# Optimization experiments

Hardware: AMD Instinct MI355X
Metric: run time of the kernel (lower is better)

Reference implementation:

```python
import jax, jax.numpy as jnp
import numpy as np

# Gating config (matches init_kwargs)
N_GROUPS = 4        # n_expert_groups
TOPK_GROUPS = 2     # n_limited_groups
TOPK = 4            # n_activated_experts
ROUTE_SCALE = 1.0


def setup_inputs() -> dict:
    key = jax.random.key(0)
    ks = jax.random.split(key, 8)
    T, D, E, I = 2048, 1024, 16, 512
    s = 0.02  # init scale for sane numerics
    return {
        "x": jax.random.normal(ks[0], (T, D), jnp.float32),
        "gate_w": jax.random.normal(ks[1], (E, D), jnp.float32) * s,
        "w1": jax.random.normal(ks[2], (E, I, D), jnp.float32) * s,
        "w2": jax.random.normal(ks[3], (E, D, I), jnp.float32) * s,
        "w3": jax.random.normal(ks[4], (E, I, D), jnp.float32) * s,
        "ws1": jax.random.normal(ks[5], (I, D), jnp.float32) * s,
        "ws2": jax.random.normal(ks[6], (D, I), jnp.float32) * s,
        "ws3": jax.random.normal(ks[7], (I, D), jnp.float32) * s,
    }


def _gate(x, gate_w):
    # GateDeepSeekV3.forward: softmax scores, group-limited routing, top-k experts.
    T = x.shape[0]
    scores = jax.nn.softmax((x @ gate_w.T).astype(jnp.float32), axis=-1)  # [T, E]
    original_scores = scores
    E = scores.shape[-1]
    # group-limited routing: keep top `TOPK_GROUPS` groups by max score (bias is None)
    s = scores.reshape(T, N_GROUPS, E // N_GROUPS)
    group_scores = s.max(axis=-1)                                  # [T, G]
    _, gidx = jax.lax.top_k(group_scores, TOPK_GROUPS)             # [T, Gk]
    mask = jnp.zeros((T, N_GROUPS), scores.dtype).at[jnp.arange(T)[:, None], gidx].set(1.0)
    s = (s * mask[:, :, None]).reshape(T, E)
    _, indices = jax.lax.top_k(s, TOPK)                            # [T, topk]
    weights = jnp.take_along_axis(original_scores, indices, axis=1) * ROUTE_SCALE
    return weights.astype(x.dtype), indices


def reference(x, gate_w, w1, w2, w3, ws1, ws2, ws3):
    T, D = x.shape
    E = w1.shape[0]
    weights, indices = _gate(x, gate_w)
    # dense [T, E] combine weights (topk indices are unique per token)
    gate_dense = jnp.zeros((T, E), x.dtype).at[jnp.arange(T)[:, None], indices].add(weights)
    # routed experts: y_t = sum_e g[t,e] * W2_e (silu(W1_e x) * (W3_e x))
    h = jax.nn.silu(jnp.einsum('td,eid->tei', x, w1)) * jnp.einsum('td,eid->tei', x, w3)
    y = jnp.einsum('tei,te,edi->td', h, gate_dense, w2)
    # shared expert MLP over all tokens
    z = (jax.nn.silu(x @ ws1.T) * (x @ ws3.T)) @ ws2.T
    return y + z
```

## Files before the change

kernel.cpp:

```cpp
#include <hip/hip_runtime.h>
#include <hip/hip_bf16.h>
#include <math.h>

typedef float v4f __attribute__((ext_vector_type(4)));
typedef short v8s __attribute__((ext_vector_type(8)));

#define T_TOK   2048
#define DDIM    1024
#define NE      16
#define IDIM    512
#define S_ROUTED 8192
#define S_ALL   10240
#define MAXTILE 104

#define OFF_TOPKI    0u
#define OFF_TOPKW    32768u
#define OFF_PART     65536u
#define OFF_CBASE    69632u
#define OFF_SEGOFF   73728u
#define OFF_NTILES   74240u
#define OFF_TROW     74752u
#define OFF_TEND     75776u
#define OFF_TEXP     76800u
#define OFF_SLOTWT   81920u
#define OFF_S2T      114688u
#define OFF_SLOTOF   155648u
#define OFF_XBF      (1u<<20)
#define OFF_H        (8u<<20)
#define OFF_YP       (24u<<20)

__device__ __forceinline__ unsigned short f2bf(float f) {
    unsigned int u = __float_as_uint(f);
    unsigned int r = (u + 0x7fffu + ((u >> 16) & 1u)) >> 16;
    return (unsigned short)r;
}
__device__ __forceinline__ float bf2f(unsigned short s) {
    return __uint_as_float((unsigned)s << 16);
}

#define GLL16(gp, lp) __builtin_amdgcn_global_load_lds( \
    (__attribute__((address_space(1))) void*)(gp), \
    (__attribute__((address_space(3))) void*)(lp), 16, 0, 0)

__global__ __launch_bounds__(256) void gate_kernel(
    const float* __restrict__ x, const float* __restrict__ gw,
    int* __restrict__ topki, float* __restrict__ topkw,
    unsigned short* __restrict__ xbf)
{
    int t = blockIdx.x;
    int tid = threadIdx.x, lane = tid & 63, wave = tid >> 6;
    const float4* xr = (const float4*)(x + (size_t)t * DDIM);
    float4 xv[4];
#pragma unroll
    for (int j = 0; j < 4; j++) xv[j] = xr[lane + 64 * j];

    __shared__ float sc[NE];
#pragma unroll
    for (int ee = 0; ee < 4; ee++) {
        int e = wave * 4 + ee;
        const float4* wr = (const float4*)(gw + (size_t)e * DDIM);
        float acc = 0.f;
#pragma unroll
        for (int j = 0; j < 4; j++) {
            float4 w = wr[lane + 64 * j];
            acc += xv[j].x * w.x + xv[j].y * w.y + xv[j].z * w.z + xv[j].w * w.w;
        }
#pragma unroll
        for (int off = 32; off; off >>= 1) acc += __shfl_down(acc, off, 64);
        if (lane == 0) sc[e] = acc;
    }
    if (wave == 0) {
#pragma unroll
        for (int j = 0; j < 4; j++) {
            int base = 4 * (lane + 64 * j);
            uint2 p;
            p.x = (unsigned)f2bf(xv[j].x) | ((unsigned)f2bf(xv[j].y) << 16);
            p.y = (unsigned)f2bf(xv[j].z) | ((unsigned)f2bf(xv[j].w) << 16);
            *(uint2*)(xbf + (size_t)t * DDIM + base) = p;
        }
    }
    __syncthreads();
    if (tid == 0) {
        float mx = sc[0];
#pragma unroll
        for (int e = 1; e < NE; e++) mx = fmaxf(mx, sc[e]);
        float sco[NE]; float sum = 0.f;
#pragma unroll
        for (int e = 0; e < NE; e++) { sco[e] = __expf(sc[e] - mx); sum += sco[e]; }
        float inv = 1.f / sum;
#pragma unroll
        for (int e = 0; e < NE; e++) sco[e] *= inv;
        float gs[4];
#pragma unroll
        for (int g = 0; g < 4; g++) {
            float m = sco[4 * g];
            m = fmaxf(m, sco[4 * g + 1]); m = fmaxf(m, sco[4 * g + 2]); m = fmaxf(m, sco[4 * g + 3]);
            gs[g] = m;
        }
        int g0 = 0;
        for (int g = 1; g < 4; g++) if (gs[g] > gs[g0]) g0 = g;
        int g1 = -1;
        for (int g = 0; g < 4; g++) { if (g == g0) continue; if (g1 < 0 || gs[g] > gs[g1]) g1 = g; }
        float ms[NE];
#pragma unroll
        for (int e = 0; e < NE; e++) {
            int g = e >> 2;
            ms[e] = (g == g0 || g == g1) ? sco[e] : 0.0f;
        }
        bool used[NE] = {false};
        for (int k = 0; k < 4; k++) {
            int best = -1;
            for (int e = 0; e < NE; e++) {
                if (used[e]) continue;
                if (best < 0 || ms[e] > ms[best]) best = e;
            }
            used[best] = true;
            topki[t * 4 + k] = best;
            topkw[t * 4 + k] = sco[best];
        }
    }
}

__global__ __launch_bounds__(256) void hist_kernel(
    const int* __restrict__ topki, int* __restrict__ part)
{
    __shared__ int cnt[16];
    int tid = threadIdx.x, b = blockIdx.x;
    if (tid < 16) cnt[tid] = 0;
    __syncthreads();
    int e = topki[b * 256 + tid];
    int lane = tid & 63;
#pragma unroll
    for (int e0 = 0; e0 < 16; e0++) {
        unsigned long long mask = __ballot(e == e0);
        if (lane == 0) atomicAdd(&cnt[e0], __popcll(mask));
    }
    __syncthreads();
    if (tid < 16) part[b * 16 + tid] = cnt[tid];
}

__global__ __launch_bounds__(256) void scan_kernel(
    const int* __restrict__ part, int* __restrict__ cbase, int* __restrict__ segoff,
    int* __restrict__ trow, int* __restrict__ tend, int* __restrict__ texp,
    int* __restrict__ ntp)
{
    int tid = threadIdx.x;
    __shared__ int tot[16];
    __shared__ int so[17];
    if (tid < 16) {
        int s = 0;
        for (int b = 0; b < 32; b++) s += part[b * 16 + tid];
        tot[tid] = s;
    }
    __syncthreads();
    if (tid == 0) {
        int off = 0;
        for (int e = 0; e < 16; e++) { so[e] = off; segoff[e] = off; off += tot[e]; }
        so[16] = off; segoff[16] = off; segoff[17] = off + T_TOK;
        int nt = 0;
        for (int e = 0; e < 17; e++) {
            int n = (e < 16) ? tot[e] : T_TOK;
            int base = (e < 16) ? so[e] : S_ROUTED;
            for (int m = 0; m < n; m += 128) {
                trow[nt] = base + m; tend[nt] = base + n; texp[nt] = e; nt++;
            }
        }
        *ntp = nt;
    }
    __syncthreads();
    if (tid < 16) {
        int run = so[tid];
        for (int b = 0; b < 32; b++) { cbase[b * 16 + tid] = run; run += part[b * 16 + tid]; }
    }
}

__global__ __launch_bounds__(256) void assign_kernel(
    const int* __restrict__ topki, const float* __restrict__ topkw,
    const int* __restrict__ cbase, int* __restrict__ s2t,
    float* __restrict__ slotwt, int* __restrict__ slotof)
{
    int b = blockIdx.x, tid = threadIdx.x;
    int i = b * 256 + tid;
    int e = topki[i];
    int lane = tid & 63, wave = tid >> 6;
    __shared__ int wcnt[4][16];
    int lrank = 0;
#pragma unroll
    for (int e0 = 0; e0 < 16; e0++) {
        unsigned long long mask = __ballot(e == e0);
        if (e == e0) lrank = __popcll(mask & ((1ull << lane) - 1ull));
        if (lane == 0) wcnt[wave][e0] = __popcll(mask);
    }
    __syncthreads();
    int pre = 0;
    for (int w = 0; w < wave; w++) pre += wcnt[w][e];
    int slot = cbase[b * 16 + e] + pre + lrank;
    int t = i >> 2;
    s2t[slot] = t;
    slotwt[slot] = topkw[i];
    slotof[i] = slot;
    if ((i & 3) == 0) s2t[S_ROUTED + t] = t;
}

__global__ __launch_bounds__(256, 3) void gemm1_kernel(
    const float* __restrict__ w1, const float* __restrict__ w3,
    const float* __restrict__ s1, const float* __restrict__ s3,
    const unsigned short* __restrict__ xbf,
    unsigned short* __restrict__ h, const float* __restrict__ slotwt,
    const int* __restrict__ s2t,
    const int* __restrict__ trow, const int* __restrict__ tend,
    const int* __restrict__ texp, const int* __restrict__ ntp)
{
    int bid = blockIdx.x;
    int tile = bid >> 3, ct = bid & 7;
    if (tile >= *ntp) return;
    int row0 = trow[tile], rend = tend[tile], e = texp[tile];
    int n0 = ct * 64;
    const float* B1 = (e < 16) ? (w1 + (size_t)e * 524288) : s1;
    const float* B3 = (e < 16) ? (w3 + (size_t)e * 524288) : s3;

    __shared__ __align__(16) short As[128 * 64];
    __shared__ __align__(16) short Bs[128 * 64];

    int tid = threadIdx.x;
    int lane = tid & 63, wave = tid >> 6;
    int wm = wave & 1, wn = wave >> 1;
    int mq = lane >> 4, nl = lane & 15;
    int rr = lane >> 3, cbl = (lane & 7) ^ rr;

    int tok[4];
#pragma unroll
    for (int j = 0; j < 4; j++)
        tok[j] = s2t[row0 + wave * 32 + j * 8 + rr];

    const float* bsrc[4];
    int brow[4], bblk[4];
#pragma unroll
    for (int j = 0; j < 4; j++) {
        int u = tid + 256 * j;
        brow[j] = u >> 3; bblk[j] = u & 7;
        int half = brow[j] >> 6;
        const float* base = half ? B3 : B1;
        bsrc[j] = base + (size_t)(n0 + (brow[j] & 63)) * DDIM + bblk[j] * 8;
    }

    v4f acc[4][4];
#pragma unroll
    for (int i = 0; i < 4; i++)
#pragma unroll
        for (int j = 0; j < 4; j++) acc[i][j] = (v4f)0.f;

    float4 br0[4], br1[4];
#pragma unroll
    for (int j = 0; j < 4; j++) {
        br0[j] = *(const float4*)(bsrc[j]);
        br1[j] = *(const float4*)(bsrc[j] + 4);
    }

    for (int ki = 0; ki < 16; ki++) {
        int kc = ki * 64;
        __syncthreads();
#pragma unroll
        for (int j = 0; j < 4; j++)
            GLL16(xbf + (size_t)tok[j] * DDIM + kc + cbl * 8, As + wave * 2048 + j * 512);
#pragma unroll
        for (int j = 0; j < 4; j++) {
            uint4 p;
            p.x = (unsigned)f2bf(br0[j].x) | ((unsigned)f2bf(br0[j].y) << 16);
            p.y = (unsigned)f2bf(br0[j].z) | ((unsigned)f2bf(br0[j].w) << 16);
            p.z = (unsigned)f2bf(br1[j].x) | ((unsigned)f2bf(br1[j].y) << 16);
            p.w = (unsigned)f2bf(br1[j].z) | ((unsigned)f2bf(br1[j].w) << 16);
            *(uint4*)(Bs + brow[j] * 64 + ((bblk[j] ^ (brow[j] & 7)) * 8)) = p;
        }
        __syncthreads();
        if (ki < 15) {
#pragma unroll
            for (int j = 0; j < 4; j++) {
                br0[j] = *(const float4*)(bsrc[j] + kc + 64);
                br1[j] = *(const float4*)(bsrc[j] + kc + 68);
            }
        }
#pragma unroll
        for (int ks = 0; ks < 2; ks++) {
            int kb = ks * 4 + mq;
            v8s a[4], b[4];
#pragma unroll
            for (int mi = 0; mi < 4; mi++) {
                int R = wm * 64 + mi * 16 + nl;
                a[mi] = *(const v8s*)(As + R * 64 + ((kb ^ (nl & 7)) * 8));
            }
#pragma unroll
            for (int ni = 0; ni < 4; ni++) {
                int S = (ni >> 1) * 64 + wn * 32 + (ni & 1) * 16 + nl;
                b[ni] = *(const v8s*)(Bs + S * 64 + ((kb ^ (nl & 7)) * 8));
            }
#pragma unroll
            for (int mi = 0; mi < 4; mi++)
#pragma unroll
                for (int ni = 0; ni < 4; ni++)
                    acc[mi][ni] = __builtin_amdgcn_mfma_f32_16x16x32_bf16(a[mi], b[ni], acc[mi][ni], 0, 0, 0);
        }
    }
#pragma unroll
    for (int mi = 0; mi < 4; mi++) {
#pragma unroll
        for (int r = 0; r < 4; r++) {
            int srow = row0 + wm * 64 + mi * 16 + mq * 4 + r;
            if (srow < rend) {
                float g = (srow < S_ROUTED) ? slotwt[srow] : 1.0f;
#pragma unroll
                for (int ni = 0; ni < 2; ni++) {
                    float p1 = acc[mi][ni][r], p3 = acc[mi][ni + 2][r];
                    float sig = 1.f / (1.f + __expf(-p1));
                    h[(size_t)srow * IDIM + n0 + wn * 32 + ni * 16 + nl] = f2bf(p1 * sig * p3 * g);
                }
            }
        }
    }
}

__global__ __launch_bounds__(256, 3) void gemm2_kernel(
    const float* __restrict__ w2, const float* __restrict__ s2w,
    const unsigned short* __restrict__ h, unsigned short* __restrict__ yp,
    const int* __restrict__ trow, const int* __restrict__ tend,
    const int* __restrict__ texp, const int* __restrict__ ntp)
{
    int bid = blockIdx.x;
    int tile = bid >> 3, ct = bid & 7;
    if (tile >= *ntp) return;
    int row0 = trow[tile], rend = tend[tile], e = texp[tile];
    int n0 = ct * 128;
    const float* B = ((e < 16) ? (w2 + (size_t)e * 524288) : s2w) + (size_t)n0 * IDIM;

    __shared__ __align__(16) short As[128 * 64];
    __shared__ __align__(16) short Bs[128 * 64];

    int tid = threadIdx.x;
    int lane = tid & 63, wave = tid >> 6;
    int wm = wave & 1, wn = wave >> 1;
    int mq = lane >> 4, nl = lane & 15;
    int rr = lane >> 3, cbl = (lane & 7) ^ rr;

    const float* bsrc[4];
    int brow[4], bblk[4];
#pragma unroll
    for (int j = 0; j < 4; j++) {
        int u = tid + 256 * j;
        brow[j] = u >> 3; bblk[j] = u & 7;
        bsrc[j] = B + (size_t)brow[j] * IDIM + bblk[j] * 8;
    }

    v4f acc[4][4];
#pragma unroll
    for (int i = 0; i < 4; i++)
#pragma unroll
        for (int j = 0; j < 4; j++) acc[i][j] = (v4f)0.f;

    float4 br0[4], br1[4];
#pragma unroll
    for (int j = 0; j < 4; j++) {
        br0[j] = *(const float4*)(bsrc[j]);
        br1[j] = *(const float4*)(bsrc[j] + 4);
    }

    for (int ki = 0; ki < 8; ki++) {
        int kc = ki * 64;
        __syncthreads();
#pragma unroll
        for (int j = 0; j < 4; j++)
            GLL16(h + (size_t)(row0 + wave * 32 + j * 8 + rr) * IDIM + kc + cbl * 8,
                  As + wave * 2048 + j * 512);
#pragma unroll
        for (int j = 0; j < 4; j++) {
            uint4 p;
            p.x = (unsigned)f2bf(br0[j].x) | ((unsigned)f2bf(br0[j].y) << 16);
            p.y = (unsigned)f2bf(br0[j].z) | ((unsigned)f2bf(br0[j].w) << 16);
            p.z = (unsigned)f2bf(br1[j].x) | ((unsigned)f2bf(br1[j].y) << 16);
            p.w = (unsigned)f2bf(br1[j].z) | ((unsigned)f2bf(br1[j].w) << 16);
            *(uint4*)(Bs + brow[j] * 64 + ((bblk[j] ^ (brow[j] & 7)) * 8)) = p;
        }
        __syncthreads();
        if (ki < 7) {
#pragma unroll
            for (int j = 0; j < 4; j++) {
                br0[j] = *(const float4*)(bsrc[j] + kc + 64);
                br1[j] = *(const float4*)(bsrc[j] + kc + 68);
            }
        }
#pragma unroll
        for (int ks = 0; ks < 2; ks++) {
            int kb = ks * 4 + mq;
            v8s a[4], b[4];
#pragma unroll
            for (int mi = 0; mi < 4; mi++) {
                int R = wm * 64 + mi * 16 + nl;
                a[mi] = *(const v8s*)(As + R * 64 + ((kb ^ (nl & 7)) * 8));
            }
#pragma unroll
            for (int ni = 0; ni < 4; ni++) {
                int S = wn * 64 + ni * 16 + nl;
                b[ni] = *(const v8s*)(Bs + S * 64 + ((kb ^ (nl & 7)) * 8));
            }
#pragma unroll
            for (int mi = 0; mi < 4; mi++)
#pragma unroll
                for (int ni = 0; ni < 4; ni++)
                    acc[mi][ni] = __builtin_amdgcn_mfma_f32_16x16x32_bf16(a[mi], b[ni], acc[mi][ni], 0, 0, 0);
        }
    }
#pragma unroll
    for (int mi = 0; mi < 4; mi++) {
#pragma unroll
        for (int r = 0; r < 4; r++) {
            int srow = row0 + wm * 64 + mi * 16 + mq * 4 + r;
            if (srow < rend) {
                unsigned short* yrow = yp + ((size_t)srow << 10) + n0 + wn * 64 + nl;
#pragma unroll
                for (int ni = 0; ni < 4; ni++)
                    yrow[ni * 16] = f2bf(acc[mi][ni][r]);
            }
        }
    }
}

__global__ __launch_bounds__(256) void combine_kernel(
    const unsigned short* __restrict__ yp, const int* __restrict__ slotof,
    float* __restrict__ out)
{
    int t = blockIdx.x;
    int c = threadIdx.x * 4;
    int s0 = slotof[t * 4 + 0], s1 = slotof[t * 4 + 1];
    int s2 = slotof[t * 4 + 2], s3 = slotof[t * 4 + 3];
    ushort4 v  = *(const ushort4*)(yp + (((size_t)(S_ROUTED + t)) << 10) + c);
    ushort4 a0 = *(const ushort4*)(yp + (((size_t)s0) << 10) + c);
    ushort4 a1 = *(const ushort4*)(yp + (((size_t)s1) << 10) + c);
    ushort4 a2 = *(const ushort4*)(yp + (((size_t)s2) << 10) + c);
    ushort4 a3 = *(const ushort4*)(yp + (((size_t)s3) << 10) + c);
    float4 o;
    o.x = bf2f(v.x) + bf2f(a0.x) + bf2f(a1.x) + bf2f(a2.x) + bf2f(a3.x);
    o.y = bf2f(v.y) + bf2f(a0.y) + bf2f(a1.y) + bf2f(a2.y) + bf2f(a3.y);
    o.z = bf2f(v.z) + bf2f(a0.z) + bf2f(a1.z) + bf2f(a2.z) + bf2f(a3.z);
    o.w = bf2f(v.w) + bf2f(a0.w) + bf2f(a1.w) + bf2f(a2.w) + bf2f(a3.w);
    *(float4*)(out + (((size_t)t) << 10) + c) = o;
}

extern "C" void kernel_launch(void* const* d_in, const int* in_sizes, int n_in,
                              void* d_out, int out_size, void* d_ws, size_t ws_size,
                              hipStream_t stream) {
    const float* x    = (const float*)d_in[0];
    const float* gw   = (const float*)d_in[1];
    const float* w1   = (const float*)d_in[2];
    const float* w2   = (const float*)d_in[3];
    const float* w3   = (const float*)d_in[4];
    const float* wsh1 = (const float*)d_in[5];
    const float* wsh2 = (const float*)d_in[6];
    const float* wsh3 = (const float*)d_in[7];
    float* out = (float*)d_out;

    char* ws = (char*)d_ws;
    int*   topki  = (int*)(ws + OFF_TOPKI);
    float* topkw  = (float*)(ws + OFF_TOPKW);
    int*   part   = (int*)(ws + OFF_PART);
    int*   cbase  = (int*)(ws + OFF_CBASE);
    int*   segoff = (int*)(ws + OFF_SEGOFF);
    int*   ntp    = (int*)(ws + OFF_NTILES);
    int*   trow   = (int*)(ws + OFF_TROW);
    int*   tend   = (int*)(ws + OFF_TEND);
    int*   texp   = (int*)(ws + OFF_TEXP);
    float* slotwt = (float*)(ws + OFF_SLOTWT);
    int*   s2t    = (int*)(ws + OFF_S2T);
    int*   slotof = (int*)(ws + OFF_SLOTOF);
    unsigned short* xbf = (unsigned short*)(ws + OFF_XBF);
    unsigned short* h   = (unsigned short*)(ws + OFF_H);
    unsigned short* yp  = (unsigned short*)(ws + OFF_YP);

    gate_kernel<<<T_TOK, 256, 0, stream>>>(x, gw, topki, topkw, xbf);
    hist_kernel<<<32, 256, 0, stream>>>(topki, part);
    scan_kernel<<<1, 256, 0, stream>>>(part, cbase, segoff, trow, tend, texp, ntp);
    assign_kernel<<<32, 256, 0, stream>>>(topki, topkw, cbase, s2t, slotwt, slotof);
    gemm1_kernel<<<MAXTILE * 8, 256, 0, stream>>>(w1, w3, wsh1, wsh3, xbf, h, slotwt, s2t,
                                                  trow, tend, texp, ntp);
    gemm2_kernel<<<MAXTILE * 8, 256, 0, stream>>>(w2, wsh2, h, yp, trow, tend, texp, ntp);
    combine_kernel<<<T_TOK, 256, 0, stream>>>(yp, slotof, out);
}
```

Before: 227.9 us.

## Pre-convert weights to bf16 and double-buffer GEMM tiles via direct LDS loads

A new kernel converts all routed and shared expert weights from fp32 to bf16 into workspace at the start of each call, using the packed bf16 convert instruction. The two GEMM kernels then load both A and B tiles straight into LDS with global_load_lds, instead of converting B in registers on every tile. The GEMM loops become a two-stage double-buffered pipeline driven by vmcnt waits and raw barriers, with launch bounds lowered to 2 blocks per CU to fit the doubled LDS. This removes repeated fp32 weight reads and per-tile conversion ALU work, at the cost of a full weight conversion pass. The bf16 w1/w3 buffers share workspace with the yp buffer, which is only safe because gemm2 runs after gemm1 has finished.

```diff
diff --git a/kernel.cpp b/kernel.cpp
--- a/kernel.cpp
+++ b/kernel.cpp
@@ -28,6 +28,12 @@
 #define OFF_XBF      (1u<<20)
 #define OFF_H        (8u<<20)
 #define OFF_YP       (24u<<20)
+#define OFF_W1BF     (24u<<20)
+#define OFF_W3BF     (40u<<20)
+#define OFF_W2BF     (56u<<20)
+#define OFF_S1BF     (72u<<20)
+#define OFF_S3BF     (73u<<20)
+#define OFF_S2BF     (74u<<20)
 
 __device__ __forceinline__ unsigned short f2bf(float f) {
     unsigned int u = __float_as_uint(f);
@@ -37,10 +43,46 @@
 __device__ __forceinline__ float bf2f(unsigned short s) {
     return __uint_as_float((unsigned)s << 16);
 }
+__device__ __forceinline__ unsigned cvt2(float lo, float hi) {
+    unsigned r;
+    asm("v_cvt_pk_bf16_f32 %0, %1, %2" : "=v"(r) : "v"(lo), "v"(hi));
+    return r;
+}
 
 #define GLL16(gp, lp) __builtin_amdgcn_global_load_lds( \
     (__attribute__((address_space(1))) void*)(gp), \
     (__attribute__((address_space(3))) void*)(lp), 16, 0, 0)
+
+__global__ __launch_bounds__(256) void wconv_kernel(
+    const float* __restrict__ w1, const float* __restrict__ w3,
+    const float* __restrict__ w2, const float* __restrict__ s1,
+    const float* __restrict__ s3, const float* __restrict__ s2,
+    unsigned short* __restrict__ o1, unsigned short* __restrict__ o3,
+    unsigned short* __restrict__ o2, unsigned short* __restrict__ os1,
+    unsigned short* __restrict__ os3, unsigned short* __restrict__ os2)
+{
+    const int BIG = 1048576;
+    const int SMALL = 65536;
+    const int total = 3 * BIG + 3 * SMALL;
+    for (int i = blockIdx.x * 256 + threadIdx.x; i < total; i += gridDim.x * 256) {
+        const float* s; unsigned short* d; int off;
+        if (i < BIG)            { s = w1; d = o1;  off = i; }
+        else if (i < 2 * BIG)   { s = w3; d = o3;  off = i - BIG; }
+        else if (i < 3 * BIG)   { s = w2; d = o2;  off = i - 2 * BIG; }
+        else {
+            int k = i - 3 * BIG;
+            if (k < SMALL)          { s = s1; d = os1; off = k; }
+            else if (k < 2 * SMALL) { s = s3; d = os3; off = k - SMALL; }
+            else                    { s = s2; d = os2; off = k - 2 * SMALL; }
+        }
+        float4 a = *(const float4*)(s + (size_t)off * 8);
+        float4 b = *(const float4*)(s + (size_t)off * 8 + 4);
+        uint4 p;
+        p.x = cvt2(a.x, a.y); p.y = cvt2(a.z, a.w);
+        p.z = cvt2(b.x, b.y); p.w = cvt2(b.z, b.w);
+        *(uint4*)(d + (size_t)off * 8) = p;
+    }
+}
 
 __global__ __launch_bounds__(256) void gate_kernel(
     const float* __restrict__ x, const float* __restrict__ gw,
@@ -202,9 +244,44 @@
     if ((i & 3) == 0) s2t[S_ROUTED + t] = t;
 }
 
-__global__ __launch_bounds__(256, 3) void gemm1_kernel(
-    const float* __restrict__ w1, const float* __restrict__ w3,
-    const float* __restrict__ s1, const float* __restrict__ s3,
+#define G1_ISSUE(T, BUF) do {                                                  \
+    _Pragma("unroll")                                                          \
+    for (int j = 0; j < 4; j++)                                                \
+        GLL16(asrc[j] + (T) * 64, (short*)As[BUF] + wave * 2048 + j * 512);    \
+    _Pragma("unroll")                                                          \
+    for (int j = 0; j < 4; j++)                                                \
+        GLL16(bsrc[j] + (T) * 64, (short*)Bs[BUF] + wave * 512 + j * 2048);    \
+} while (0)
+
+#define G1_COMP(BUF) do {                                                      \
+    const short* Ac = (const short*)As[BUF];                                   \
+    const short* Bc = (const short*)Bs[BUF];                                   \
+    _Pragma("unroll")                                                          \
+    for (int ks = 0; ks < 2; ks++) {                                           \
+        int kb = ks * 4 + mq;                                                  \
+        v8s a[4], b[4];                                                        \
+        _Pragma("unroll")                                                      \
+        for (int mi = 0; mi < 4; mi++) {                                       \
+            int R = wm * 64 + mi * 16 + nl;                                    \
+            a[mi] = *(const v8s*)(Ac + R * 64 + ((kb ^ (nl & 7)) * 8));        \
+        }                                                                      \
+        _Pragma("unroll")                                                      \
+        for (int ni = 0; ni < 4; ni++) {                                       \
+            int S = (ni >> 1) * 64 + wn * 32 + (ni & 1) * 16 + nl;             \
+            b[ni] = *(const v8s*)(Bc + S * 64 + ((kb ^ (nl & 7)) * 8));        \
+        }                                                                      \
+        _Pragma("unroll")                                                      \
+        for (int mi = 0; mi < 4; mi++)                                         \
+            _Pragma("unroll")                                                  \
+            for (int ni = 0; ni < 4; ni++)                                     \
+                acc[mi][ni] = __builtin_amdgcn_mfma_f32_16x16x32_bf16(         \
+                    a[mi], b[ni], acc[mi][ni], 0, 0, 0);                       \
+    }                                                                          \
+} while (0)
+
+__global__ __launch_bounds__(256, 2) void gemm1_kernel(
+    const unsigned short* __restrict__ w1bf, const unsigned short* __restrict__ w3bf,
+    const unsigned short* __restrict__ s1bf, const unsigned short* __restrict__ s3bf,
     const unsigned short* __restrict__ xbf,
     unsigned short* __restrict__ h, const float* __restrict__ slotwt,
     const int* __restrict__ s2t,
@@ -216,32 +293,30 @@
     if (tile >= *ntp) return;
     int row0 = trow[tile], rend = tend[tile], e = texp[tile];
     int n0 = ct * 64;
-    const float* B1 = (e < 16) ? (w1 + (size_t)e * 524288) : s1;
-    const float* B3 = (e < 16) ? (w3 + (size_t)e * 524288) : s3;
-
-    __shared__ __align__(16) short As[128 * 64];
-    __shared__ __align__(16) short Bs[128 * 64];
+    const unsigned short* B1 = (e < 16) ? (w1bf + (size_t)e * 524288) : s1bf;
+    const unsigned short* B3 = (e < 16) ? (w3bf + (size_t)e * 524288) : s3bf;
+
+    __shared__ __align__(16) short As[2][128 * 64];
+    __shared__ __align__(16) short Bs[2][128 * 64];
 
     int tid = threadIdx.x;
     int lane = tid & 63, wave = tid >> 6;
     int wm = wave & 1, wn = wave >> 1;
     int mq = lane >> 4, nl = lane & 15;
-    int rr = lane >> 3, cbl = (lane & 7) ^ rr;
-
-    int tok[4];
+    int rr = lane >> 3, s7 = lane & 7;
+    int swz = (s7 ^ rr) * 8;
+
+    const unsigned short* asrc[4];
 #pragma unroll
     for (int j = 0; j < 4; j++)
-        tok[j] = s2t[row0 + wave * 32 + j * 8 + rr];
-
-    const float* bsrc[4];
-    int brow[4], bblk[4];
+        asrc[j] = xbf + (size_t)s2t[row0 + wave * 32 + j * 8 + rr] * DDIM + swz;
+
+    const unsigned short* bsrc[4];
 #pragma unroll
     for (int j = 0; j < 4; j++) {
-        int u = tid + 256 * j;
-        brow[j] = u >> 3; bblk[j] = u & 7;
-        int half = brow[j] >> 6;
-        const float* base = half ? B3 : B1;
-        bsrc[j] = base + (size_t)(n0 + (brow[j] & 63)) * DDIM + bblk[j] * 8;
+        int R = wave * 8 + j * 32 + rr;
+        const unsigned short* base = (R >> 6) ? B3 : B1;
+        bsrc[j] = base + (size_t)(n0 + (R & 63)) * DDIM + swz;
     }
 
     v4f acc[4][4];
@@ -250,57 +325,19 @@
 #pragma unroll
         for (int j = 0; j < 4; j++) acc[i][j] = (v4f)0.f;
 
-    float4 br0[4], br1[4];
-#pragma unroll
-    for (int j = 0; j < 4; j++) {
-        br0[j] = *(const float4*)(bsrc[j]);
-        br1[j] = *(const float4*)(bsrc[j] + 4);
-    }
-
-    for (int ki = 0; ki < 16; ki++) {
-        int kc = ki * 64;
-        __syncthreads();
-#pragma unroll
-        for (int j = 0; j < 4; j++)
-            GLL16(xbf + (size_t)tok[j] * DDIM + kc + cbl * 8, As + wave * 2048 + j * 512);
-#pragma unroll
-        for (int j = 0; j < 4; j++) {
-            uint4 p;
-            p.x = (unsigned)f2bf(br0[j].x) | ((unsigned)f2bf(br0[j].y) << 16);
-            p.y = (unsigned)f2bf(br0[j].z) | ((unsigned)f2bf(br0[j].w) << 16);
-            p.z = (unsigned)f2bf(br1[j].x) | ((unsigned)f2bf(br1[j].y) << 16);
-            p.w = (unsigned)f2bf(br1[j].z) | ((unsigned)f2bf(br1[j].w) << 16);
-            *(uint4*)(Bs + brow[j] * 64 + ((bblk[j] ^ (brow[j] & 7)) * 8)) = p;
-        }
-        __syncthreads();
-        if (ki < 15) {
-#pragma unroll
-            for (int j = 0; j < 4; j++) {
-                br0[j] = *(const float4*)(bsrc[j] + kc + 64);
-                br1[j] = *(const float4*)(bsrc[j] + kc + 68);
-            }
-        }
-#pragma unroll
-        for (int ks = 0; ks < 2; ks++) {
-            int kb = ks * 4 + mq;
-            v8s a[4], b[4];
-#pragma unroll
-            for (int mi = 0; mi < 4; mi++) {
-                int R = wm * 64 + mi * 16 + nl;
-                a[mi] = *(const v8s*)(As + R * 64 + ((kb ^ (nl & 7)) * 8));
-            }
-#pragma unroll
-            for (int ni = 0; ni < 4; ni++) {
-                int S = (ni >> 1) * 64 + wn * 32 + (ni & 1) * 16 + nl;
-                b[ni] = *(const v8s*)(Bs + S * 64 + ((kb ^ (nl & 7)) * 8));
-            }
-#pragma unroll
-            for (int mi = 0; mi < 4; mi++)
-#pragma unroll
-                for (int ni = 0; ni < 4; ni++)
-                    acc[mi][ni] = __builtin_amdgcn_mfma_f32_16x16x32_bf16(a[mi], b[ni], acc[mi][ni], 0, 0, 0);
-        }
-    }
+    G1_ISSUE(0, 0);
+    G1_ISSUE(1, 1);
+    for (int ki = 0; ki < 15; ki++) {
+        asm volatile("s_waitcnt vmcnt(8)" ::: "memory");
+        __builtin_amdgcn_s_barrier();
+        G1_COMP(ki & 1);
+        __builtin_amdgcn_s_barrier();
+        if (ki < 14) G1_ISSUE(ki + 2, ki & 1);
+    }
+    asm volatile("s_waitcnt vmcnt(0)" ::: "memory");
+    __builtin_amdgcn_s_barrier();
+    G1_COMP(1);
+
 #pragma unroll
     for (int mi = 0; mi < 4; mi++) {
 #pragma unroll
@@ -319,8 +356,43 @@
     }
 }
 
-__global__ __launch_bounds__(256, 3) void gemm2_kernel(
-    const float* __restrict__ w2, const float* __restrict__ s2w,
+#define G2_ISSUE(T, BUF) do {                                                  \
+    _Pragma("unroll")                                                          \
+    for (int j = 0; j < 4; j++)                                                \
+        GLL16(asrc[j] + (T) * 64, (short*)As[BUF] + wave * 2048 + j * 512);    \
+    _Pragma("unroll")                                                          \
+    for (int j = 0; j < 4; j++)                                                \
+        GLL16(bsrc[j] + (T) * 64, (short*)Bs[BUF] + wave * 512 + j * 2048);    \
+} while (0)
+
+#define G2_COMP(BUF) do {                                                      \
+    const short* Ac = (const short*)As[BUF];                                   \
+    const short* Bc = (const short*)Bs[BUF];                                   \
+    _Pragma("unroll")                                                          \
+    for (int ks = 0; ks < 2; ks++) {                                           \
+        int kb = ks * 4 + mq;                                                  \
+        v8s a[4], b[4];                                                        \
+        _Pragma("unroll")                                                      \
+        for (int mi = 0; mi < 4; mi++) {                                       \
+            int R = wm * 64 + mi * 16 + nl;                                    \
+            a[mi] = *(const v8s*)(Ac + R * 64 + ((kb ^ (nl & 7)) * 8));        \
+        }                                                                      \
+        _Pragma("unroll")                                                      \
+        for (int ni = 0; ni < 4; ni++) {                                       \
+            int S = wn * 64 + ni * 16 + nl;                                    \
+            b[ni] = *(const v8s*)(Bc + S * 64 + ((kb ^ (nl & 7)) * 8));        \
+        }                                                                      \
+        _Pragma("unroll")                                                      \
+        for (int mi = 0; mi < 4; mi++)                                         \
+            _Pragma("unroll")                                                  \
+            for (int ni = 0; ni < 4; ni++)                                     \
+                acc[mi][ni] = __builtin_amdgcn_mfma_f32_16x16x32_bf16(         \
+                    a[mi], b[ni], acc[mi][ni], 0, 0, 0);                       \
+    }                                                                          \
+} while (0)
+
+__global__ __launch_bounds__(256, 2) void gemm2_kernel(
+    const unsigned short* __restrict__ w2bf, const unsigned short* __restrict__ s2bf,
     const unsigned short* __restrict__ h, unsigned short* __restrict__ yp,
     const int* __restrict__ trow, const int* __restrict__ tend,
     const int* __restrict__ texp, const int* __restrict__ ntp)
@@ -330,24 +402,28 @@
     if (tile >= *ntp) return;
     int row0 = trow[tile], rend = tend[tile], e = texp[tile];
     int n0 = ct * 128;
-    const float* B = ((e < 16) ? (w2 + (size_t)e * 524288) : s2w) + (size_t)n0 * IDIM;
-
-    __shared__ __align__(16) short As[128 * 64];
-    __shared__ __align__(16) short Bs[128 * 64];
+    const unsigned short* B = ((e < 16) ? (w2bf + (size_t)e * 524288) : s2bf) + (size_t)n0 * IDIM;
+
+    __shared__ __align__(16) short As[2][128 * 64];
+    __shared__ __align__(16) short Bs[2][128 * 64];
 
     int tid = threadIdx.x;
     int lane = tid & 63, wave = tid >> 6;
     int wm = wave & 1, wn = wave >> 1;
     int mq = lane >> 4, nl = lane & 15;
-    int rr = lane >> 3, cbl = (lane & 7) ^ rr;
-
-    const float* bsrc[4];
-    int brow[4], bblk[4];
+    int rr = lane >> 3, s7 = lane & 7;
+    int swz = (s7 ^ rr) * 8;
+
+    const unsigned short* asrc[4];
+#pragma unroll
+    for (int j = 0; j < 4; j++)
+        asrc[j] = h + (size_t)(row0 + wave * 32 + j * 8 + rr) * IDIM + swz;
+
+    const unsigned short* bsrc[4];
 #pragma unroll
     for (int j = 0; j < 4; j++) {
-        int u = tid + 256 * j;
-        brow[j] = u >> 3; bblk[j] = u & 7;
-        bsrc[j] = B + (size_t)brow[j] * IDIM + bblk[j] * 8;
+        int R = wave * 8 + j * 32 + rr;
+        bsrc[j] = B + (size_t)R * IDIM + swz;
     }
 
     v4f acc[4][4];
@@ -356,58 +432,19 @@
 #pragma unroll
         for (int j = 0; j < 4; j++) acc[i][j] = (v4f)0.f;
 
-    float4 br0[4], br1[4];
-#pragma unroll
-    for (int j = 0; j < 4; j++) {
-        br0[j] = *(const float4*)(bsrc[j]);
-        br1[j] = *(const float4*)(bsrc[j] + 4);
-    }
-
-    for (int ki = 0; ki < 8; ki++) {
-        int kc = ki * 64;
-        __syncthreads();
-#pragma unroll
-        for (int j = 0; j < 4; j++)
-            GLL16(h + (size_t)(row0 + wave * 32 + j * 8 + rr) * IDIM + kc + cbl * 8,
-                  As + wave * 2048 + j * 512);
-#pragma unroll
-        for (int j = 0; j < 4; j++) {
-            uint4 p;
-            p.x = (unsigned)f2bf(br0[j].x) | ((unsigned)f2bf(br0[j].y) << 16);
-            p.y = (unsigned)f2bf(br0[j].z) | ((unsigned)f2bf(br0[j].w) << 16);
-            p.z = (unsigned)f2bf(br1[j].x) | ((unsigned)f2bf(br1[j].y) << 16);
-            p.w = (unsigned)f2bf(br1[j].z) | ((unsigned)f2bf(br1[j].w) << 16);
-            *(uint4*)(Bs + brow[j] * 64 + ((bblk[j] ^ (brow[j] & 7)) * 8)) = p;
-        }
-        __syncthreads();
-        if (ki < 7) {
-#pragma unroll
-            for (int j = 0; j < 4; j++) {
-                br0[j] = *(const float4*)(bsrc[j] + kc + 64);
-                br1[j] = *(const float4*)(bsrc[j] + kc + 68);
-            }
-        }
-#pragma unroll
-        for (int ks = 0; ks < 2; ks++) {
-            int kb = ks * 4 + mq;
-            v8s a[4], b[4];
-#pragma unroll
-            for (int mi = 0; mi < 4; mi++) {
-                int R = wm * 64 + mi * 16 + nl;
-                a[mi] = *(const v8s*)(As + R * 64 + ((kb ^ (nl & 7)) * 8));
-            }
-#pragma unroll
-            for (int ni = 0; ni < 4; ni++) {
-                int S = wn * 64 + ni * 16 + nl;
-                b[ni] = *(const v8s*)(Bs + S * 64 + ((kb ^ (nl & 7)) * 8));
-            }
-#pragma unroll
-            for (int mi = 0; mi < 4; mi++)
-#pragma unroll
-                for (int ni = 0; ni < 4; ni++)
-                    acc[mi][ni] = __builtin_amdgcn_mfma_f32_16x16x32_bf16(a[mi], b[ni], acc[mi][ni], 0, 0, 0);
-        }
-    }
+    G2_ISSUE(0, 0);
+    G2_ISSUE(1, 1);
+    for (int ki = 0; ki < 7; ki++) {
+        asm volatile("s_waitcnt vmcnt(8)" ::: "memory");
+        __builtin_amdgcn_s_barrier();
+        G2_COMP(ki & 1);
+        __builtin_amdgcn_s_barrier();
+        if (ki < 6) G2_ISSUE(ki + 2, ki & 1);
+    }
+    asm volatile("s_waitcnt vmcnt(0)" ::: "memory");
+    __builtin_amdgcn_s_barrier();
+    G2_COMP(1);
+
 #pragma unroll
     for (int mi = 0; mi < 4; mi++) {
 #pragma unroll
@@ -470,16 +507,24 @@
     float* slotwt = (float*)(ws + OFF_SLOTWT);
     int*   s2t    = (int*)(ws + OFF_S2T);
     int*   slotof = (int*)(ws + OFF_SLOTOF);
-    unsigned short* xbf = (unsigned short*)(ws + OFF_XBF);
-    unsigned short* h   = (unsigned short*)(ws + OFF_H);
-    unsigned short* yp  = (unsigned short*)(ws + OFF_YP);
-
+    unsigned short* xbf  = (unsigned short*)(ws + OFF_XBF);
+    unsigned short* h    = (unsigned short*)(ws + OFF_H);
+    unsigned short* yp   = (unsigned short*)(ws + OFF_YP);
+    unsigned short* w1bf = (unsigned short*)(ws + OFF_W1BF);
+    unsigned short* w3bf = (unsigned short*)(ws + OFF_W3BF);
+    unsigned short* w2bf = (unsigned short*)(ws + OFF_W2BF);
+    unsigned short* s1bf = (unsigned short*)(ws + OFF_S1BF);
+    unsigned short* s3bf = (unsigned short*)(ws + OFF_S3BF);
+    unsigned short* s2bf = (unsigned short*)(ws + OFF_S2BF);
+
+    wconv_kernel<<<4096, 256, 0, stream>>>(w1, w3, w2, wsh1, wsh3, wsh2,
+                                           w1bf, w3bf, w2bf, s1bf, s3bf, s2bf);
     gate_kernel<<<T_TOK, 256, 0, stream>>>(x, gw, topki, topkw, xbf);
     hist_kernel<<<32, 256, 0, stream>>>(topki, part);
     scan_kernel<<<1, 256, 0, stream>>>(part, cbase, segoff, trow, tend, texp, ntp);
     assign_kernel<<<32, 256, 0, stream>>>(topki, topkw, cbase, s2t, slotwt, slotof);
-    gemm1_kernel<<<MAXTILE * 8, 256, 0, stream>>>(w1, w3, wsh1, wsh3, xbf, h, slotwt, s2t,
+    gemm1_kernel<<<MAXTILE * 8, 256, 0, stream>>>(w1bf, w3bf, s1bf, s3bf, xbf, h, slotwt, s2t,
                                                   trow, tend, texp, ntp);
-    gemm2_kernel<<<MAXTILE * 8, 256, 0, stream>>>(w2, wsh2, h, yp, trow, tend, texp, ntp);
+    gemm2_kernel<<<MAXTILE * 8, 256, 0, stream>>>(w2bf, s2bf, h, yp, trow, tend, texp, ntp);
     combine_kernel<<<T_TOK, 256, 0, stream>>>(yp, slotof, out);
 }
```

New measurement: 242.4 us. 1.06x slower.
